# Kernel tuning notes

Measured on AMD Instinct MI355X. Metric: run time of the kernel, lower is better.

The kernel has to match this reference:

```python
import jax, jax.numpy as jnp
import numpy as np

HID = 256
NUM_EMB = 30
MAX_LEN = 500  # decode steps = MAX_LEN + 1


def setup_inputs() -> dict:
    key = jax.random.key(0)
    ks = jax.random.split(key, 20)
    B, C, H, W = 64, 512, 32, 32
    s = 0.05
    d = {}
    d["fea"] = jax.random.normal(ks[0], (B, C, H, W), jnp.float32)
    d["targets"] = jax.random.randint(ks[1], (B, MAX_LEN + 1), 0, NUM_EMB)
    d["i2h_w"] = jax.random.normal(ks[2], (C, HID), jnp.float32) * s
    d["h2h_w"] = jax.random.normal(ks[3], (HID, HID), jnp.float32) * s
    d["h2h_b"] = jax.random.normal(ks[4], (HID,), jnp.float32) * s
    d["score_w"] = jax.random.normal(ks[5], (HID, 1), jnp.float32) * s
    d["gru_w_ih"] = jax.random.normal(ks[6], (C + NUM_EMB, 3 * HID), jnp.float32) * s
    d["gru_w_hh"] = jax.random.normal(ks[7], (HID, 3 * HID), jnp.float32) * s
    d["gru_b_ih"] = jax.random.normal(ks[8], (3 * HID,), jnp.float32) * s
    d["gru_b_hh"] = jax.random.normal(ks[9], (3 * HID,), jnp.float32) * s
    d["sg1_w"] = jax.random.normal(ks[10], (HID, HID), jnp.float32) * s
    d["sg1_b"] = jax.random.normal(ks[11], (HID,), jnp.float32) * s
    d["sg2_w"] = jax.random.normal(ks[12], (HID, NUM_EMB), jnp.float32) * s
    d["sg2_b"] = jax.random.normal(ks[13], (NUM_EMB,), jnp.float32) * s
    d["lg1_w"] = jax.random.normal(ks[14], (HID, HID), jnp.float32) * s
    d["lg1_b"] = jax.random.normal(ks[15], (HID,), jnp.float32) * s
    d["lg2_w"] = jax.random.normal(ks[16], (HID, 4), jnp.float32) * s
    d["lg2_b"] = jax.random.normal(ks[17], (4,), jnp.float32) * s
    return d


def reference(fea, targets, i2h_w, h2h_w, h2h_b, score_w,
              gru_w_ih, gru_w_hh, gru_b_ih, gru_b_hh,
              sg1_w, sg1_b, sg2_w, sg2_b, lg1_w, lg1_b, lg2_w, lg2_b):
    B, C, H, W = fea.shape
    feat = fea.reshape(B, C, H * W).transpose(0, 2, 1)          # [B,T,C]
    # content projection of encoder features is step-invariant: hoist out of loop
    proj = jnp.einsum('btc,ch->bth', feat, i2h_w)               # [B,T,HID]

    def step(hidden, char):
        # attention over spatial positions
        ph = hidden @ h2h_w + h2h_b                             # [B,HID]
        e = jnp.tanh(proj + ph[:, None, :]) @ score_w           # [B,T,1]
        alpha = jax.nn.softmax(e[..., 0], axis=1)               # [B,T]
        context = jnp.einsum('bt,btc->bc', alpha, feat)         # [B,C]
        onehot = jax.nn.one_hot(char, NUM_EMB, dtype=hidden.dtype)
        x = jnp.concatenate([context, onehot], axis=-1)         # [B,C+NUM_EMB]
        # GRU cell (torch semantics)
        gx = x @ gru_w_ih + gru_b_ih
        gh = hidden @ gru_w_hh + gru_b_hh
        xr, xz, xn = jnp.split(gx, 3, axis=-1)
        hr, hz, hn = jnp.split(gh, 3, axis=-1)
        r = jax.nn.sigmoid(xr + hr)
        z = jax.nn.sigmoid(xz + hz)
        n = jnp.tanh(xn + r * hn)
        h_new = (1.0 - z) * n + z * hidden
        struct = (h_new @ sg1_w + sg1_b) @ sg2_w + sg2_b        # [B,NUM_EMB]
        loc = jax.nn.sigmoid((h_new @ lg1_w + lg1_b) @ lg2_w + lg2_b)  # [B,4]
        return h_new, (struct, loc)

    h0 = jnp.zeros((B, HID), fea.dtype)
    _, (structs, locs) = jax.lax.scan(step, h0, targets.T)      # over 501 steps
    structure_preds = structs.transpose(1, 0, 2)                # [B,501,NUM_EMB]
    loc_preds = locs.transpose(1, 0, 2)                         # [B,501,4]
    return structure_preds, loc_preds
```

## Files before the change

### kernel.cpp

```cpp
#include <hip/hip_runtime.h>
#include <hip/hip_bf16.h>
#include <hip/hip_fp16.h>
#include <math.h>

#define BB 64
#define CDIM 512
#define TT 1024
#define HID 256
#define NEMB 30
#define GDIM 768

typedef _Float16 v2h __attribute__((ext_vector_type(2)));

struct TanhC { float c[7]; };

__device__ inline float f_dot2(v2h a, v2h b, float c) {
  return __builtin_amdgcn_fdot2(a, b, c, false);
}
__device__ inline v2h u2v(unsigned u) { return __builtin_bit_cast(v2h, u); }
__device__ inline unsigned v2u(v2h h) { return __builtin_bit_cast(unsigned, h); }
__device__ inline unsigned packh2(float a, float b) {
  v2h t = {(_Float16)a, (_Float16)b};
  return v2u(t);
}
__device__ inline v2h v2splat(float f) {
  _Float16 h = (_Float16)f;
  v2h r = {h, h};
  return r;
}

__device__ inline float ldin(const void* p, long i, int isb) {
  if (isb) {
    unsigned u = ((const unsigned short*)p)[i];
    return __uint_as_float(u << 16);
  }
  return ((const float*)p)[i];
}

template <int CTRL, int RM, int BM, bool BC>
__device__ inline float dpp_add(float v) {
  int m = __builtin_amdgcn_update_dpp(0, __builtin_bit_cast(int, v), CTRL, RM, BM, BC);
  return v + __builtin_bit_cast(float, m);
}
__device__ inline float wave_sum64(float v) {
  v = dpp_add<0x111, 0xf, 0xf, true>(v);
  v = dpp_add<0x112, 0xf, 0xf, true>(v);
  v = dpp_add<0x114, 0xf, 0xe, false>(v);
  v = dpp_add<0x118, 0xf, 0xc, false>(v);
  v = dpp_add<0x142, 0xa, 0xf, false>(v);
  v = dpp_add<0x143, 0xc, 0xf, false>(v);
  return v;
}

__global__ void k_sniff(const void* fea, int* flag) {
  __shared__ int s[256];
  int tid = threadIdx.x;
  const unsigned short* u16 = (const unsigned short*)fea;
  int cnt = 0;
  for (int i = tid; i < 2048; i += 256) {
    unsigned u = u16[2 * i];
    float v = __uint_as_float(u << 16);
    float a = fabsf(v);
    if (a > 1e-6f && a < 16.0f) cnt++;
  }
  s[tid] = cnt;
  __syncthreads();
  for (int off = 128; off > 0; off >>= 1) {
    if (tid < off) s[tid] += s[tid + off];
    __syncthreads();
  }
  if (tid == 0) flag[0] = (s[0] > 1024) ? 1 : 0;
}

__global__ void k_cvt_f(const void* src, float* dst, long n, const int* flag) {
  int isb = flag[0];
  long i = (long)blockIdx.x * blockDim.x + threadIdx.x;
  long stride = (long)gridDim.x * blockDim.x;
  for (; i < n; i += stride) dst[i] = ldin(src, i, isb);
}

__global__ void k_wc(const void* i2h, const void* wih, unsigned* wc2, const int* flag) {
  int isb = flag[0];
  int idx = blockIdx.x * 256 + threadIdx.x;
  int cp = idx >> 10, col = idx & 1023;
  float a, b;
  if (col < 256) {
    a = ldin(i2h, (long)(2 * cp) * 256 + col, isb);
    b = ldin(i2h, (long)(2 * cp + 1) * 256 + col, isb);
  } else {
    int j = col - 256;
    a = ldin(wih, (long)(2 * cp) * GDIM + j, isb);
    b = ldin(wih, (long)(2 * cp + 1) * GDIM + j, isb);
  }
  wc2[idx] = packh2(a, b);
}

__global__ void k_w4(const void* h2hw, const void* whhw, unsigned* w4, const int* flag) {
  int isb = flag[0];
  int idx = blockIdx.x * 256 + threadIdx.x;
  int l = idx >> 10, col = idx & 1023;
  float a, b2;
  if (col < 256) {
    a = ldin(h2hw, (long)(2 * l) * 256 + col, isb);
    b2 = ldin(h2hw, (long)(2 * l + 1) * 256 + col, isb);
  } else {
    int j = col - 256;
    a = ldin(whhw, (long)(2 * l) * GDIM + j, isb);
    b2 = ldin(whhw, (long)(2 * l + 1) * GDIM + j, isb);
  }
  w4[idx] = packh2(a, b2);
}

__global__ void k_bias4(const void* h2hb, const void* bhh, float* bias4, const int* flag) {
  int isb = flag[0];
  int col = blockIdx.x * 256 + threadIdx.x;
  bias4[col] = (col < 256) ? ldin(h2hb, col, isb) : ldin(bhh, col - 256, isb);
}

__global__ void k_embb(const void* wih, const void* bih, float* embb, const int* flag) {
  int isb = flag[0];
  int idx = blockIdx.x * 256 + threadIdx.x;
  if (idx >= NEMB * GDIM) return;
  int e = idx / GDIM, col = idx % GDIM;
  embb[idx] = ldin(wih, (long)(512 + e) * GDIM + col, isb) + ldin(bih, col, isb);
}

__global__ void k_comb(const void* sg1w, const void* sg1b, const void* sg2w, const void* sg2b,
                       const void* lg1w, const void* lg1b, const void* lg2w, const void* lg2b,
                       float* comb_w, float* comb_b, const int* flag) {
  int isb = flag[0];
  int tid = threadIdx.x;
  float acc[34];
#pragma unroll
  for (int o = 0; o < 34; ++o) acc[o] = 0.f;
  for (int m = 0; m < HID; ++m) {
    float s1 = ldin(sg1w, (long)tid * HID + m, isb);
    float l1 = ldin(lg1w, (long)tid * HID + m, isb);
#pragma unroll
    for (int o = 0; o < 30; ++o) acc[o] += s1 * ldin(sg2w, (long)m * NEMB + o, isb);
#pragma unroll
    for (int o = 0; o < 4; ++o) acc[30 + o] += l1 * ldin(lg2w, (long)m * 4 + o, isb);
  }
  for (int o = 0; o < 34; ++o) comb_w[tid * 34 + o] = acc[o];
  if (tid < 34) {
    float a = 0.f;
    if (tid < 30) {
      for (int m = 0; m < HID; ++m) a += ldin(sg1b, m, isb) * ldin(sg2w, (long)m * NEMB + tid, isb);
      a += ldin(sg2b, tid, isb);
    } else {
      int o = tid - 30;
      for (int m = 0; m < HID; ++m) a += ldin(lg1b, m, isb) * ldin(lg2w, (long)m * 4 + o, isb);
      a += ldin(lg2b, o, isb);
    }
    comb_b[tid] = a;
  }
}

__global__ __launch_bounds__(256) void k_gemm(const void* fea, const unsigned* wc2,
                                              unsigned* proj2, unsigned* fw2, const int* flag) {
  const int isb = flag[0];
  const int blk = blockIdx.x;
  const int b = blk >> 6;
  const int tt = (blk >> 3) & 7;
  const int cc = blk & 7;
  const int t0 = tt * 128, c0 = cc * 128;
  __shared__ __align__(16) unsigned At[32][136];
  __shared__ __align__(16) unsigned Wt[32][136];
  const int tid = threadIdx.x;
  const int cp_l = tid >> 3, sg = tid & 7;
  const int tm = tid & 15, tn = tid >> 4;
  float acc[8][8];
#pragma unroll
  for (int i = 0; i < 8; ++i)
#pragma unroll
    for (int jj = 0; jj < 8; ++jj) acc[i][jj] = 0.f;

  for (int kt = 0; kt < 8; ++kt) {
    const int crow = (kt * 32 + cp_l) * 2;
    if (isb) {
      const unsigned short* f0p =
          (const unsigned short*)fea + ((long)b * CDIM + crow) * TT + t0 + sg * 16;
      const unsigned short* f1p = f0p + TT;
#pragma unroll
      for (int q = 0; q < 2; ++q) {
        ushort4 u0a = ((const ushort4*)f0p)[2 * q];
        ushort4 u0b = ((const ushort4*)f0p)[2 * q + 1];
        ushort4 u1a = ((const ushort4*)f1p)[2 * q];
        ushort4 u1b = ((const ushort4*)f1p)[2 * q + 1];
        unsigned short a0[8] = {u0a.x, u0a.y, u0a.z, u0a.w, u0b.x, u0b.y, u0b.z, u0b.w};
        unsigned short a1[8] = {u1a.x, u1a.y, u1a.z, u1a.w, u1b.x, u1b.y, u1b.z, u1b.w};
#pragma unroll
        for (int e = 0; e < 8; ++e) {
          float f0 = __uint_as_float(((unsigned)a0[e]) << 16);
          float f1 = __uint_as_float(((unsigned)a1[e]) << 16);
          At[cp_l][sg * 16 + q * 8 + e] = packh2(f0, f1);
        }
      }
    } else {
      const float* f0p = (const float*)fea + ((long)b * CDIM + crow) * TT + t0 + sg * 16;
      const float* f1p = f0p + TT;
#pragma unroll
      for (int q = 0; q < 4; ++q) {
        float4 v0 = ((const float4*)f0p)[q];
        float4 v1 = ((const float4*)f1p)[q];
        At[cp_l][sg * 16 + q * 4 + 0] = packh2(v0.x, v1.x);
        At[cp_l][sg * 16 + q * 4 + 1] = packh2(v0.y, v1.y);
        At[cp_l][sg * 16 + q * 4 + 2] = packh2(v0.z, v1.z);
        At[cp_l][sg * 16 + q * 4 + 3] = packh2(v0.w, v1.w);
      }
    }
    {
      const uint4* wp = (const uint4*)(wc2 + (long)(kt * 32 + cp_l) * 1024 + c0 + sg * 16);
#pragma unroll
      for (int q = 0; q < 4; ++q) {
        uint4 w = wp[q];
        Wt[cp_l][sg * 16 + q * 4 + 0] = w.x;
        Wt[cp_l][sg * 16 + q * 4 + 1] = w.y;
        Wt[cp_l][sg * 16 + q * 4 + 2] = w.z;
        Wt[cp_l][sg * 16 + q * 4 + 3] = w.w;
      }
    }
    __syncthreads();
    for (int cp = 0; cp < 32; ++cp) {
      uint4 aq0 = *(const uint4*)&At[cp][tm * 4];
      uint4 aq1 = *(const uint4*)&At[cp][64 + tm * 4];
      uint4 bq0 = *(const uint4*)&Wt[cp][tn * 4];
      uint4 bq1 = *(const uint4*)&Wt[cp][64 + tn * 4];
      unsigned av[8] = {aq0.x, aq0.y, aq0.z, aq0.w, aq1.x, aq1.y, aq1.z, aq1.w};
      unsigned bv[8] = {bq0.x, bq0.y, bq0.z, bq0.w, bq1.x, bq1.y, bq1.z, bq1.w};
#pragma unroll
      for (int ti = 0; ti < 8; ++ti)
#pragma unroll
        for (int ci = 0; ci < 8; ++ci)
          acc[ti][ci] = f_dot2(u2v(av[ti]), u2v(bv[ci]), acc[ti][ci]);
    }
    __syncthreads();
  }

#pragma unroll
  for (int q = 0; q < 2; ++q) {
    const int tq = t0 + q * 64 + tm * 4;
#pragma unroll
    for (int pr = 0; pr < 2; ++pr) {
      const int tp = (tq >> 1) + pr;
      const int r0 = q * 4 + 2 * pr, r1 = r0 + 1;
      if (cc < 2) {
#pragma unroll
        for (int ci = 0; ci < 8; ++ci) {
          int h = c0 + tn * 4 + (ci & 3) + ((ci >> 2) << 6);
          proj2[((long)b * HID + h) * 512 + tp] = packh2(acc[r0][ci], acc[r1][ci]);
        }
      } else {
        unsigned* row = fw2 + ((long)b * 512 + tp) * GDIM + (c0 - 256) + tn * 4;
        uint4 pa = {packh2(acc[r0][0], acc[r1][0]), packh2(acc[r0][1], acc[r1][1]),
                    packh2(acc[r0][2], acc[r1][2]), packh2(acc[r0][3], acc[r1][3])};
        uint4 pb = {packh2(acc[r0][4], acc[r1][4]), packh2(acc[r0][5], acc[r1][5]),
                    packh2(acc[r0][6], acc[r1][6]), packh2(acc[r0][7], acc[r1][7])};
        *(uint4*)row = pa;
        *(uint4*)(row + 64) = pb;
      }
    }
  }
}

__global__ __launch_bounds__(1024) void k_main_c(
    const unsigned* proj2, const unsigned* fw2, const int* targets, const unsigned* w4,
    const float* bias4, const float* embb, const float* scoref, const float* comb_w,
    const float* comb_b, void* out, const int* flag, int steps, TanhC tc, int* bar1, int* bar2,
    float* Sx, float* ghxx, float* gxpx) {
  const int tid = threadIdx.x;
  const int g = blockIdx.x & 63;
  const int j = blockIdx.x >> 6;
  const int lane = tid & 63, wid = tid >> 6;
  const int isb = flag[0];

  __shared__ float sh_pa[3072];
  __shared__ unsigned sh_phsc[HID];
  __shared__ unsigned sh_alpha2[128];
  __shared__ float sh_hidden[HID];
  __shared__ unsigned sh_h2[128];
  __shared__ float sh_red[16];

  float my_sc = (tid < HID) ? scoref[tid] : 0.f;
  if (tid < HID) sh_hidden[tid] = 0.f;
  if (tid < 128) sh_h2[tid] = 0u;
  __syncthreads();

  const v2h C0 = v2splat(tc.c[0]), C1 = v2splat(tc.c[1]), C2 = v2splat(tc.c[2]),
            C3 = v2splat(tc.c[3]), C4 = v2splat(tc.c[4]), C5 = v2splat(tc.c[5]),
            C6 = v2splat(tc.c[6]);
  const v2h CLO = v2splat(-3.9f), CHI = v2splat(3.9f);
  const v2h VS = v2splat(0.0625f);

  const unsigned* pbase = proj2 + (long)g * HID * 512 + j * 128;
  const unsigned* fwbase = fw2 + ((long)g * 512 + j * 128) * GDIM;

  for (int step = 0; step < steps; ++step) {
    const int tgt = targets[g * steps + step];
    const int par = step & 1;
    float* S_cur = Sx + par * 256;
    float* ghx_cur = ghxx + (long)par * 64 * GDIM;
    float* gxp_cur = gxpx + (long)par * 64 * 4 * GDIM;

    {
      const int chunk = tid >> 8, col = tid & 255;
      float a = 0.f;
      const unsigned* wp = w4 + (long)(chunk * 32) * 1024 + col;
#pragma unroll 8
      for (int l = 0; l < 32; ++l) a = f_dot2(u2v(sh_h2[chunk * 32 + l]), u2v(wp[l * 1024]), a);
      sh_pa[chunk * 256 + col] = a;
    }
    if (tid < 768) {
      const int ch = tid / 192, cl = tid % 192;
      const int gcol = 256 + j * 192 + cl;
      float a = 0.f;
      const unsigned* wp = w4 + (long)(ch * 32) * 1024 + gcol;
#pragma unroll 8
      for (int l = 0; l < 32; ++l) a = f_dot2(u2v(sh_h2[ch * 32 + l]), u2v(wp[l * 1024]), a);
      sh_pa[1024 + ch * 192 + cl] = a;
    }
    __syncthreads();
    if (tid < 256) {
      float ph = sh_pa[tid] + sh_pa[256 + tid] + sh_pa[512 + tid] + sh_pa[768 + tid] + bias4[tid];
      sh_phsc[tid] = packh2(ph, my_sc);
    } else if (tid < 448) {
      int cl = tid - 256;
      float gv = sh_pa[1024 + cl] + sh_pa[1024 + 192 + cl] + sh_pa[1024 + 384 + cl] +
                 sh_pa[1024 + 576 + cl] + bias4[256 + j * 192 + cl];
      ghx_cur[(long)g * GDIM + j * 192 + cl] = gv;
    }
    __syncthreads();

    {
      const int hh = tid >> 7, tpl = tid & 127;
      const unsigned* pb = pbase + tpl;
      v2h acc = v2splat(0.f);
      float f0 = 0.f, f1 = 0.f;
#pragma unroll 8
      for (int hi = 0; hi < 32; ++hi) {
        int h = hh * 32 + hi;
        v2h ps = u2v(sh_phsc[h]);
        v2h phb = {ps.x, ps.x};
        v2h scb = {ps.y, ps.y};
        v2h x = u2v(pb[(long)h * 512]) + phb;
        x = __builtin_elementwise_max(x, CLO);
        x = __builtin_elementwise_min(x, CHI);
        v2h v = x * x * VS;
        v2h p = C6;
        p = p * v + C5;
        p = p * v + C4;
        p = p * v + C3;
        p = p * v + C2;
        p = p * v + C1;
        p = p * v + C0;
        acc = acc + scb * (p * x);
      }
      f0 = (float)acc.x;
      f1 = (float)acc.y;
      sh_pa[(hh * 128 + tpl) * 2] = f0;
      sh_pa[(hh * 128 + tpl) * 2 + 1] = f1;
    }
    __syncthreads();
    float p0 = 0.f, p1 = 0.f;
    if (tid < 128) {
      float e0 = 0.f, e1 = 0.f;
#pragma unroll
      for (int hh = 0; hh < 8; ++hh) {
        e0 += sh_pa[(hh * 128 + tid) * 2];
        e1 += sh_pa[(hh * 128 + tid) * 2 + 1];
      }
      p0 = exp2f(e0 * 1.44269504f);
      p1 = exp2f(e1 * 1.44269504f);
      float s = wave_sum64(p0 + p1);
      if (lane == 63) sh_red[wid] = s;
    }
    __syncthreads();
    if (tid == 0) S_cur[g * 4 + j] = sh_red[0] + sh_red[1];

    __syncthreads();
    if (tid == 0) {
      __hip_atomic_fetch_add(&bar1[g], 1, __ATOMIC_ACQ_REL, __HIP_MEMORY_SCOPE_AGENT);
      const int tgt4 = 4 * (step + 1);
      while (__hip_atomic_load(&bar1[g], __ATOMIC_RELAXED, __HIP_MEMORY_SCOPE_AGENT) < tgt4)
        __builtin_amdgcn_s_sleep(2);
      (void)__hip_atomic_load(&bar1[g], __ATOMIC_ACQUIRE, __HIP_MEMORY_SCOPE_AGENT);
    }
    __syncthreads();
    if (tid < 128) {
      float D = S_cur[g * 4] + S_cur[g * 4 + 1] + S_cur[g * 4 + 2] + S_cur[g * 4 + 3];
      float rs = 1.0f / D;
      sh_alpha2[tid] = packh2(p0 * rs, p1 * rs);
    }
    __syncthreads();

    if (tid < 768) {
      const int sub = tid / 192, cg = tid % 192;
      const int c4 = cg * 4;
      const uint4* fr = (const uint4*)(fwbase + (long)(sub * 32) * GDIM + c4);
      float a0 = 0.f, a1 = 0.f, a2 = 0.f, a3 = 0.f;
#pragma unroll 4
      for (int i = 0; i < 32; ++i) {
        v2h al = u2v(sh_alpha2[sub * 32 + i]);
        uint4 w = fr[(long)i * 192];
        a0 = f_dot2(al, u2v(w.x), a0);
        a1 = f_dot2(al, u2v(w.y), a1);
        a2 = f_dot2(al, u2v(w.z), a2);
        a3 = f_dot2(al, u2v(w.w), a3);
      }
      *(float4*)&sh_pa[sub * GDIM + c4] = make_float4(a0, a1, a2, a3);
    }
    __syncthreads();
    if (tid < 768) {
      float v = sh_pa[tid] + sh_pa[GDIM + tid] + sh_pa[2 * GDIM + tid] + sh_pa[3 * GDIM + tid];
      gxp_cur[((long)g * 4 + j) * GDIM + tid] = v;
    }

    __syncthreads();
    if (tid == 0) {
      __hip_atomic_fetch_add(&bar2[g], 1, __ATOMIC_ACQ_REL, __HIP_MEMORY_SCOPE_AGENT);
      const int tgt4 = 4 * (step + 1);
      while (__hip_atomic_load(&bar2[g], __ATOMIC_RELAXED, __HIP_MEMORY_SCOPE_AGENT) < tgt4)
        __builtin_amdgcn_s_sleep(2);
      (void)__hip_atomic_load(&bar2[g], __ATOMIC_ACQUIRE, __HIP_MEMORY_SCOPE_AGENT);
    }
    __syncthreads();

    if (tid < 256) {
      const float* eb = embb + (long)tgt * GDIM;
      float gr = eb[tid], gz = eb[tid + 256], gn = eb[tid + 512];
#pragma unroll
      for (int jj = 0; jj < 4; ++jj) {
        const float* gp = gxp_cur + ((long)g * 4 + jj) * GDIM;
        gr += gp[tid];
        gz += gp[tid + 256];
        gn += gp[tid + 512];
      }
      const float* gh = ghx_cur + (long)g * GDIM;
      float hr = gh[tid], hz = gh[tid + 256], hn = gh[tid + 512];
      float r = 1.f / (1.f + __expf(-(gr + hr)));
      float z = 1.f / (1.f + __expf(-(gz + hz)));
      float n = tanhf(gn + r * hn);
      sh_hidden[tid] = (1.f - z) * n + z * sh_hidden[tid];
    }
    __syncthreads();

    if (tid < 128) sh_h2[tid] = packh2(sh_hidden[2 * tid], sh_hidden[2 * tid + 1]);
    if (j == (step & 3)) {
      float hv[4];
      if (tid < 64) {
#pragma unroll
        for (int k = 0; k < 4; ++k) hv[k] = sh_hidden[lane + 64 * k];
      }
      if (tid < 34) {
        float a = comb_b[tid];
#pragma unroll
        for (int k = 0; k < 4; ++k) {
          for (int l = 0; l < 64; ++l) {
            float h = __builtin_bit_cast(
                float, __builtin_amdgcn_readlane(__builtin_bit_cast(int, hv[k]), l));
            a += h * comb_w[(64 * k + l) * 34 + tid];
          }
        }
        long so;
        float vv;
        if (tid < 30) {
          so = ((long)g * steps + step) * 30 + tid;
          vv = a;
        } else {
          so = (long)BB * steps * 30 + ((long)g * steps + step) * 4 + (tid - 30);
          vv = 1.f / (1.f + __expf(-a));
        }
        if (isb)
          ((__hip_bfloat16*)out)[so] = __float2bfloat16(vv);
        else
          ((float*)out)[so] = vv;
      }
    }
    __syncthreads();
  }
}

static void fit_tanh(float cf[7]) {
  double A[7][7] = {{0}}, r[7] = {0};
  const int N = 1024;
  for (int i = 1; i <= N; ++i) {
    double x = 3.9 * i / N;
    double v = (x * x) / 16.0;
    double t = tanh(x);
    double phi[7];
    double pw = x;
    for (int jj = 0; jj < 7; ++jj) {
      phi[jj] = pw;
      pw *= v;
    }
    for (int jj = 0; jj < 7; ++jj) {
      r[jj] += phi[jj] * t;
      for (int k = 0; k < 7; ++k) A[jj][k] += phi[jj] * phi[k];
    }
  }
  for (int col = 0; col < 7; ++col) {
    int piv = col;
    for (int rr = col + 1; rr < 7; ++rr)
      if (fabs(A[rr][col]) > fabs(A[piv][col])) piv = rr;
    if (piv != col) {
      for (int k = 0; k < 7; ++k) {
        double tmp = A[col][k];
        A[col][k] = A[piv][k];
        A[piv][k] = tmp;
      }
      double tb = r[col];
      r[col] = r[piv];
      r[piv] = tb;
    }
    double d = A[col][col];
    for (int rr = col + 1; rr < 7; ++rr) {
      double f = A[rr][col] / d;
      for (int k = col; k < 7; ++k) A[rr][k] -= f * A[col][k];
      r[rr] -= f * r[col];
    }
  }
  double c[7];
  for (int col = 6; col >= 0; --col) {
    double ss = r[col];
    for (int k = col + 1; k < 7; ++k) ss -= A[col][k] * c[k];
    c[col] = ss / A[col][col];
  }
  for (int jj = 0; jj < 7; ++jj) cf[jj] = (float)c[jj];
}

extern "C" void kernel_launch(void* const* d_in, const int* in_sizes, int n_in, void* d_out,
                              int out_size, void* d_ws, size_t ws_size, hipStream_t stream) {
  (void)n_in;
  (void)out_size;
  (void)ws_size;
  const void* fea = d_in[0];
  const int* targets = (const int*)d_in[1];
  const void* i2h_w = d_in[2];
  const void* h2h_w = d_in[3];
  const void* h2h_b = d_in[4];
  const void* score_w = d_in[5];
  const void* gru_w_ih = d_in[6];
  const void* gru_w_hh = d_in[7];
  const void* gru_b_ih = d_in[8];
  const void* gru_b_hh = d_in[9];
  const void* sg1_w = d_in[10];
  const void* sg1_b = d_in[11];
  const void* sg2_w = d_in[12];
  const void* sg2_b = d_in[13];
  const void* lg1_w = d_in[14];
  const void* lg1_b = d_in[15];
  const void* lg2_w = d_in[16];
  const void* lg2_b = d_in[17];
  const int steps = in_sizes[1] / BB;

  char* p = (char*)d_ws;
  auto alloc = [&](size_t bytes) {
    char* r = p;
    p += (bytes + 255) & ~(size_t)255;
    return r;
  };
  unsigned* proj2 = (unsigned*)alloc((size_t)BB * HID * 512 * 4);
  unsigned* fw2 = (unsigned*)alloc((size_t)BB * 512 * GDIM * 4);
  unsigned* wc2 = (unsigned*)alloc((size_t)256 * 1024 * 4);
  unsigned* w4 = (unsigned*)alloc((size_t)128 * 1024 * 4);
  float* bias4 = (float*)alloc(1024 * 4);
  float* embb = (float*)alloc((size_t)NEMB * GDIM * 4);
  float* scoref = (float*)alloc(256 * 4);
  float* combw = (float*)alloc(256 * 34 * 4);
  float* combb = (float*)alloc(64 * 4);
  int* flag = (int*)alloc(256);
  int* bars = (int*)alloc(4096);
  float* Sx = (float*)alloc((size_t)2 * 64 * 4 * 4);
  float* ghxx = (float*)alloc((size_t)2 * 64 * GDIM * 4);
  float* gxpx = (float*)alloc((size_t)2 * 64 * 4 * GDIM * 4);
  int* bar1 = bars;
  int* bar2 = bars + 64;

  TanhC tc;
  fit_tanh(tc.c);

  hipMemsetAsync(bars, 0, 4096, stream);
  k_sniff<<<1, 256, 0, stream>>>(fea, flag);
  k_wc<<<1024, 256, 0, stream>>>(i2h_w, gru_w_ih, wc2, flag);
  k_w4<<<512, 256, 0, stream>>>(h2h_w, gru_w_hh, w4, flag);
  k_bias4<<<4, 256, 0, stream>>>(h2h_b, gru_b_hh, bias4, flag);
  k_embb<<<90, 256, 0, stream>>>(gru_w_ih, gru_b_ih, embb, flag);
  k_cvt_f<<<1, 256, 0, stream>>>(score_w, scoref, 256, flag);
  k_comb<<<1, 256, 0, stream>>>(sg1_w, sg1_b, sg2_w, sg2_b, lg1_w, lg1_b, lg2_w, lg2_b, combw,
                                combb, flag);
  k_gemm<<<4096, 256, 0, stream>>>(fea, wc2, proj2, fw2, flag);

  k_main_c<<<256, 1024, 0, stream>>>(proj2, fw2, targets, w4, bias4, embb, scoref, combw, combb,
                                     d_out, flag, steps, tc, bar1, bar2, Sx, ghxx, gxpx);
}
```

Before: 25.19 ms.

## Defer softmax normalization to drop a grid barrier and transpose projection layout

The context product now runs on unnormalized exponentials, and the division by the softmax sum is applied later inside the GRU gate step. This removes the second per-step cross-block barrier, so each step waits on one barrier instead of two. The projection tensor is stored time-major so each thread reads contiguous uint4 rows in the tanh-score loop, and the first feature rows are prefetched into registers before the matvec. The price is more register pressure, a padded shared layout, and fp16 accumulation of unnormalized weights, which could overflow or lose precision.

```diff
diff --git a/kernel.cpp b/kernel.cpp
--- a/kernel.cpp
+++ b/kernel.cpp
@@ -157,7 +157,7 @@
 }
 
 __global__ __launch_bounds__(256) void k_gemm(const void* fea, const unsigned* wc2,
-                                              unsigned* proj2, unsigned* fw2, const int* flag) {
+                                              unsigned* pp, unsigned* fw2, const int* flag) {
   const int isb = flag[0];
   const int blk = blockIdx.x;
   const int b = blk >> 6;
@@ -244,42 +244,38 @@
     for (int pr = 0; pr < 2; ++pr) {
       const int tp = (tq >> 1) + pr;
       const int r0 = q * 4 + 2 * pr, r1 = r0 + 1;
-      if (cc < 2) {
-#pragma unroll
-        for (int ci = 0; ci < 8; ++ci) {
-          int h = c0 + tn * 4 + (ci & 3) + ((ci >> 2) << 6);
-          proj2[((long)b * HID + h) * 512 + tp] = packh2(acc[r0][ci], acc[r1][ci]);
-        }
-      } else {
-        unsigned* row = fw2 + ((long)b * 512 + tp) * GDIM + (c0 - 256) + tn * 4;
-        uint4 pa = {packh2(acc[r0][0], acc[r1][0]), packh2(acc[r0][1], acc[r1][1]),
-                    packh2(acc[r0][2], acc[r1][2]), packh2(acc[r0][3], acc[r1][3])};
-        uint4 pb = {packh2(acc[r0][4], acc[r1][4]), packh2(acc[r0][5], acc[r1][5]),
-                    packh2(acc[r0][6], acc[r1][6]), packh2(acc[r0][7], acc[r1][7])};
-        *(uint4*)row = pa;
-        *(uint4*)(row + 64) = pb;
-      }
-    }
-  }
-}
-
-__global__ __launch_bounds__(1024) void k_main_c(
-    const unsigned* proj2, const unsigned* fw2, const int* targets, const unsigned* w4,
+      unsigned* row;
+      if (cc < 2)
+        row = pp + ((long)b * 512 + tp) * 256 + c0 + tn * 4;
+      else
+        row = fw2 + ((long)b * 512 + tp) * GDIM + (c0 - 256) + tn * 4;
+      uint4 pa = {packh2(acc[r0][0], acc[r1][0]), packh2(acc[r0][1], acc[r1][1]),
+                  packh2(acc[r0][2], acc[r1][2]), packh2(acc[r0][3], acc[r1][3])};
+      uint4 pb = {packh2(acc[r0][4], acc[r1][4]), packh2(acc[r0][5], acc[r1][5]),
+                  packh2(acc[r0][6], acc[r1][6]), packh2(acc[r0][7], acc[r1][7])};
+      *(uint4*)row = pa;
+      *(uint4*)(row + 64) = pb;
+    }
+  }
+}
+
+__global__ __launch_bounds__(1024, 4) void k_main_c2(
+    const unsigned* pp, const unsigned* fw2, const int* targets, const unsigned* w4,
     const float* bias4, const float* embb, const float* scoref, const float* comb_w,
-    const float* comb_b, void* out, const int* flag, int steps, TanhC tc, int* bar1, int* bar2,
-    float* Sx, float* ghxx, float* gxpx) {
+    const float* comb_b, void* out, const int* flag, int steps, TanhC tc, int* bar1, float* Sx,
+    float* ghxx, float* gxpx) {
   const int tid = threadIdx.x;
   const int g = blockIdx.x & 63;
   const int j = blockIdx.x >> 6;
   const int lane = tid & 63, wid = tid >> 6;
   const int isb = flag[0];
 
-  __shared__ float sh_pa[3072];
-  __shared__ unsigned sh_phsc[HID];
+  __shared__ __align__(16) float sh_pa[3072];
+  __shared__ unsigned sh_phsc[264];
   __shared__ unsigned sh_alpha2[128];
   __shared__ float sh_hidden[HID];
   __shared__ unsigned sh_h2[128];
-  __shared__ float sh_red[16];
+  __shared__ float sh_red[4];
 
   float my_sc = (tid < HID) ? scoref[tid] : 0.f;
   if (tid < HID) sh_hidden[tid] = 0.f;
@@ -292,8 +288,15 @@
   const v2h CLO = v2splat(-3.9f), CHI = v2splat(3.9f);
   const v2h VS = v2splat(0.0625f);
 
-  const unsigned* pbase = proj2 + (long)g * HID * 512 + j * 128;
+  const unsigned* ppbase = pp + ((long)g * 512 + j * 128) * 256;
   const unsigned* fwbase = fw2 + ((long)g * 512 + j * 128) * GDIM;
+
+  const int dsub = (tid < 768) ? tid / 192 : 0;
+  const int dcg = (tid < 768) ? tid % 192 : 0;
+  const uint4* frbase = (const uint4*)(fwbase + (long)(dsub * 32) * GDIM) + dcg;
+
+  const int btp = tid >> 3, bhc = tid & 7;
+  const uint4* prow = (const uint4*)(ppbase + (long)btp * 256) + bhc * 8;
 
   for (int step = 0; step < steps; ++step) {
     const int tgt = targets[g * steps + step];
@@ -301,6 +304,10 @@
     float* S_cur = Sx + par * 256;
     float* ghx_cur = ghxx + (long)par * 64 * GDIM;
     float* gxp_cur = gxpx + (long)par * 64 * 4 * GDIM;
+
+    uint4 pf[8];
+#pragma unroll
+    for (int i = 0; i < 8; ++i) pf[i] = frbase[(long)i * 192];
 
     {
       const int chunk = tid >> 8, col = tid & 255;
@@ -322,7 +329,7 @@
     __syncthreads();
     if (tid < 256) {
       float ph = sh_pa[tid] + sh_pa[256 + tid] + sh_pa[512 + tid] + sh_pa[768 + tid] + bias4[tid];
-      sh_phsc[tid] = packh2(ph, my_sc);
+      sh_phsc[(tid >> 5) * 33 + (tid & 31)] = packh2(ph, my_sc);
     } else if (tid < 448) {
       int cl = tid - 256;
       float gv = sh_pa[1024 + cl] + sh_pa[1024 + 192 + cl] + sh_pa[1024 + 384 + cl] +
@@ -332,50 +339,78 @@
     __syncthreads();
 
     {
-      const int hh = tid >> 7, tpl = tid & 127;
-      const unsigned* pb = pbase + tpl;
       v2h acc = v2splat(0.f);
-      float f0 = 0.f, f1 = 0.f;
-#pragma unroll 8
-      for (int hi = 0; hi < 32; ++hi) {
-        int h = hh * 32 + hi;
-        v2h ps = u2v(sh_phsc[h]);
-        v2h phb = {ps.x, ps.x};
-        v2h scb = {ps.y, ps.y};
-        v2h x = u2v(pb[(long)h * 512]) + phb;
-        x = __builtin_elementwise_max(x, CLO);
-        x = __builtin_elementwise_min(x, CHI);
-        v2h v = x * x * VS;
-        v2h p = C6;
-        p = p * v + C5;
-        p = p * v + C4;
-        p = p * v + C3;
-        p = p * v + C2;
-        p = p * v + C1;
-        p = p * v + C0;
-        acc = acc + scb * (p * x);
-      }
-      f0 = (float)acc.x;
-      f1 = (float)acc.y;
-      sh_pa[(hh * 128 + tpl) * 2] = f0;
-      sh_pa[(hh * 128 + tpl) * 2 + 1] = f1;
-    }
-    __syncthreads();
-    float p0 = 0.f, p1 = 0.f;
+#pragma unroll
+      for (int q = 0; q < 8; ++q) {
+        uint4 w = prow[q];
+        unsigned we[4] = {w.x, w.y, w.z, w.w};
+#pragma unroll
+        for (int e = 0; e < 4; ++e) {
+          int hl = q * 4 + e;
+          v2h ps = u2v(sh_phsc[bhc * 33 + hl]);
+          v2h phb = {ps.x, ps.x};
+          v2h scb = {ps.y, ps.y};
+          v2h x = u2v(we[e]) + phb;
+          x = __builtin_elementwise_max(x, CLO);
+          x = __builtin_elementwise_min(x, CHI);
+          v2h v = x * x * VS;
+          v2h p = C6;
+          p = p * v + C5;
+          p = p * v + C4;
+          p = p * v + C3;
+          p = p * v + C2;
+          p = p * v + C1;
+          p = p * v + C0;
+          acc = acc + scb * (p * x);
+        }
+      }
+      ((float2*)sh_pa)[btp * 9 + bhc] = make_float2((float)acc.x, (float)acc.y);
+    }
+    __syncthreads();
+
     if (tid < 128) {
       float e0 = 0.f, e1 = 0.f;
 #pragma unroll
-      for (int hh = 0; hh < 8; ++hh) {
-        e0 += sh_pa[(hh * 128 + tid) * 2];
-        e1 += sh_pa[(hh * 128 + tid) * 2 + 1];
-      }
-      p0 = exp2f(e0 * 1.44269504f);
-      p1 = exp2f(e1 * 1.44269504f);
+      for (int k = 0; k < 8; ++k) {
+        float2 v = ((const float2*)sh_pa)[tid * 9 + k];
+        e0 += v.x;
+        e1 += v.y;
+      }
+      float p0 = exp2f(e0 * 1.44269504f);
+      float p1 = exp2f(e1 * 1.44269504f);
+      sh_alpha2[tid] = packh2(p0, p1);
       float s = wave_sum64(p0 + p1);
       if (lane == 63) sh_red[wid] = s;
     }
     __syncthreads();
     if (tid == 0) S_cur[g * 4 + j] = sh_red[0] + sh_red[1];
+
+    if (tid < 768) {
+      float a0 = 0.f, a1 = 0.f, a2 = 0.f, a3 = 0.f;
+#pragma unroll
+      for (int i = 0; i < 8; ++i) {
+        v2h al = u2v(sh_alpha2[dsub * 32 + i]);
+        a0 = f_dot2(al, u2v(pf[i].x), a0);
+        a1 = f_dot2(al, u2v(pf[i].y), a1);
+        a2 = f_dot2(al, u2v(pf[i].z), a2);
+        a3 = f_dot2(al, u2v(pf[i].w), a3);
+      }
+#pragma unroll 8
+      for (int i = 8; i < 32; ++i) {
+        uint4 w = frbase[(long)i * 192];
+        v2h al = u2v(sh_alpha2[dsub * 32 + i]);
+        a0 = f_dot2(al, u2v(w.x), a0);
+        a1 = f_dot2(al, u2v(w.y), a1);
+        a2 = f_dot2(al, u2v(w.z), a2);
+        a3 = f_dot2(al, u2v(w.w), a3);
+      }
+      *(float4*)&sh_pa[dsub * GDIM + dcg * 4] = make_float4(a0, a1, a2, a3);
+    }
+    __syncthreads();
+    if (tid < 768) {
+      float v = sh_pa[tid] + sh_pa[GDIM + tid] + sh_pa[2 * GDIM + tid] + sh_pa[3 * GDIM + tid];
+      gxp_cur[((long)g * 4 + j) * GDIM + tid] = v;
+    }
 
     __syncthreads();
     if (tid == 0) {
@@ -386,48 +421,12 @@
       (void)__hip_atomic_load(&bar1[g], __ATOMIC_ACQUIRE, __HIP_MEMORY_SCOPE_AGENT);
     }
     __syncthreads();
-    if (tid < 128) {
+
+    if (tid < 256) {
       float D = S_cur[g * 4] + S_cur[g * 4 + 1] + S_cur[g * 4 + 2] + S_cur[g * 4 + 3];
       float rs = 1.0f / D;
-      sh_alpha2[tid] = packh2(p0 * rs, p1 * rs);
-    }
-    __syncthreads();
-
-    if (tid < 768) {
-      const int sub = tid / 192, cg = tid % 192;
-      const int c4 = cg * 4;
-      const uint4* fr = (const uint4*)(fwbase + (long)(sub * 32) * GDIM + c4);
-      float a0 = 0.f, a1 = 0.f, a2 = 0.f, a3 = 0.f;
-#pragma unroll 4
-      for (int i = 0; i < 32; ++i) {
-        v2h al = u2v(sh_alpha2[sub * 32 + i]);
-        uint4 w = fr[(long)i * 192];
-        a0 = f_dot2(al, u2v(w.x), a0);
-        a1 = f_dot2(al, u2v(w.y), a1);
-        a2 = f_dot2(al, u2v(w.z), a2);
-        a3 = f_dot2(al, u2v(w.w), a3);
-      }
-      *(float4*)&sh_pa[sub * GDIM + c4] = make_float4(a0, a1, a2, a3);
-    }
-    __syncthreads();
-    if (tid < 768) {
-      float v = sh_pa[tid] + sh_pa[GDIM + tid] + sh_pa[2 * GDIM + tid] + sh_pa[3 * GDIM + tid];
-      gxp_cur[((long)g * 4 + j) * GDIM + tid] = v;
-    }
-
-    __syncthreads();
-    if (tid == 0) {
-      __hip_atomic_fetch_add(&bar2[g], 1, __ATOMIC_ACQ_REL, __HIP_MEMORY_SCOPE_AGENT);
-      const int tgt4 = 4 * (step + 1);
-      while (__hip_atomic_load(&bar2[g], __ATOMIC_RELAXED, __HIP_MEMORY_SCOPE_AGENT) < tgt4)
-        __builtin_amdgcn_s_sleep(2);
-      (void)__hip_atomic_load(&bar2[g], __ATOMIC_ACQUIRE, __HIP_MEMORY_SCOPE_AGENT);
-    }
-    __syncthreads();
-
-    if (tid < 256) {
       const float* eb = embb + (long)tgt * GDIM;
-      float gr = eb[tid], gz = eb[tid + 256], gn = eb[tid + 512];
+      float gr = 0.f, gz = 0.f, gn = 0.f;
 #pragma unroll
       for (int jj = 0; jj < 4; ++jj) {
         const float* gp = gxp_cur + ((long)g * 4 + jj) * GDIM;
@@ -435,6 +434,9 @@
         gz += gp[tid + 256];
         gn += gp[tid + 512];
       }
+      gr = gr * rs + eb[tid];
+      gz = gz * rs + eb[tid + 256];
+      gn = gn * rs + eb[tid + 512];
       const float* gh = ghx_cur + (long)g * GDIM;
       float hr = gh[tid], hz = gh[tid + 256], hn = gh[tid + 512];
       float r = 1.f / (1.f + __expf(-(gr + hr)));
@@ -559,7 +561,7 @@
     p += (bytes + 255) & ~(size_t)255;
     return r;
   };
-  unsigned* proj2 = (unsigned*)alloc((size_t)BB * HID * 512 * 4);
+  unsigned* pp = (unsigned*)alloc((size_t)BB * 512 * 256 * 4);
   unsigned* fw2 = (unsigned*)alloc((size_t)BB * 512 * GDIM * 4);
   unsigned* wc2 = (unsigned*)alloc((size_t)256 * 1024 * 4);
   unsigned* w4 = (unsigned*)alloc((size_t)128 * 1024 * 4);
@@ -574,7 +576,6 @@
   float* ghxx = (float*)alloc((size_t)2 * 64 * GDIM * 4);
   float* gxpx = (float*)alloc((size_t)2 * 64 * 4 * GDIM * 4);
   int* bar1 = bars;
-  int* bar2 = bars + 64;
 
   TanhC tc;
   fit_tanh(tc.c);
@@ -588,8 +589,8 @@
   k_cvt_f<<<1, 256, 0, stream>>>(score_w, scoref, 256, flag);
   k_comb<<<1, 256, 0, stream>>>(sg1_w, sg1_b, sg2_w, sg2_b, lg1_w, lg1_b, lg2_w, lg2_b, combw,
                                 combb, flag);
-  k_gemm<<<4096, 256, 0, stream>>>(fea, wc2, proj2, fw2, flag);
-
-  k_main_c<<<256, 1024, 0, stream>>>(proj2, fw2, targets, w4, bias4, embb, scoref, combw, combb,
-                                     d_out, flag, steps, tc, bar1, bar2, Sx, ghxx, gxpx);
-}
+  k_gemm<<<4096, 256, 0, stream>>>(fea, wc2, pp, fw2, flag);
+
+  k_main_c2<<<256, 1024, 0, stream>>>(pp, fw2, targets, w4, bias4, embb, scoref, combw, combb,
+                                      d_out, flag, steps, tc, bar1, Sx, ghxx, gxpx);
+}
```

New measurement: 21.72 ms. 13.8% less time.
